# Kernel tuning notes

Hardware: AMD Instinct MI355X
Metric: run time of the kernel (lower is better)

Reference implementation:

```python
import jax, jax.numpy as jnp
import numpy as np

B, C, H, W = 4, 64, 64, 64
CI = C // 2  # inter_channels


def setup_inputs() -> dict:
    key = jax.random.key(0)
    k1, k2, k3, k4, k5 = jax.random.split(key, 5)
    x = jax.random.normal(k1, (B, C, H, W), dtype=jnp.float32)
    # 1x1 conv g: in C -> CI (weight [CI, C], bias [CI])
    Wg = jax.random.normal(k2, (CI, C), dtype=jnp.float32) * (1.0 / np.sqrt(C))
    bg = jax.random.normal(k3, (CI,), dtype=jnp.float32) * 0.01
    # 1x1 conv W_z: CI -> C
    Wz = jax.random.normal(k4, (C, CI), dtype=jnp.float32) * (1.0 / np.sqrt(CI))
    bz = jax.random.normal(k5, (C,), dtype=jnp.float32) * 0.01
    return {"x": x, "Wg": Wg, "bg": bg, "Wz": Wz, "bz": bz}


def reference(x, Wg, bg, Wz, bz):
    b, c, h, w = x.shape
    n = h * w
    xf = x.reshape(b, c, n)                       # [B,C,N]
    # g projection (1x1 conv) then flatten: [B,N,CI]
    g_x = jnp.einsum('bcn,oc->bno', xf, Wg) + bg  # [B,N,CI]
    # theta = phi = raw x flattened
    theta = xf.transpose(0, 2, 1)                 # [B,N,C]
    f = jnp.einsum('bnc,bcm->bnm', theta, xf)     # [B,N,N]
    f_div_C = jax.nn.softmax(f, axis=-1)
    y = jnp.einsum('bnm,bmo->bno', f_div_C, g_x)  # [B,N,CI]
    y = y.transpose(0, 2, 1).reshape(b, CI, h, w)  # [B,CI,H,W]
    # W_z projection (1x1 conv) + residual
    W_y = jnp.einsum('oi,bihw->bohw', Wz, y) + bz[None, :, None, None]
    return W_y + x
```

## Files before the change

### kernel.cpp

```cpp
#include <hip/hip_runtime.h>
#include <hip/hip_bf16.h>
#include <math.h>

#define B_  4
#define C_  64
#define N_  4096
#define CI_ 32
#define L2E 1.4426950408889634f

typedef __attribute__((ext_vector_type(8))) unsigned short u16x8;
typedef __attribute__((ext_vector_type(8))) __bf16        bf16x8;
typedef __attribute__((ext_vector_type(4))) float         f32x4;

union bfu { u16x8 u; bf16x8 b; };

__device__ __forceinline__ unsigned short f2bf(float f) {
    union { float f; unsigned int i; } v; v.f = f;
    unsigned int r = v.i + 0x7FFFu + ((v.i >> 16) & 1u);
    return (unsigned short)(r >> 16);
}

__global__ __launch_bounds__(256) void k_prep(
    const float* __restrict__ x, const float* __restrict__ Wg,
    const float* __restrict__ bg, unsigned short* __restrict__ xT,
    unsigned short* __restrict__ gx, float* __restrict__ diagS)
{
    __shared__ __align__(16) float tile[64][68];
    __shared__ float part[4][64][33];
    const int t  = threadIdx.x;
    const int b  = blockIdx.x >> 6;
    const int n0 = (blockIdx.x & 63) * 64;

    #pragma unroll
    for (int pass = 0; pass < 4; ++pass) {
        int c   = (t >> 4) + pass * 16;
        int nl4 = (t & 15) * 4;
        float4 v = *(const float4*)(x + (size_t)(b * C_ + c) * N_ + n0 + nl4);
        *(float4*)&tile[c][nl4] = v;
    }
    __syncthreads();

    {
        const int n  = t >> 2;
        const int cc = (t & 3) * 16;
        u16x8 a, b2;
        #pragma unroll
        for (int j = 0; j < 8; ++j) {
            a[j]  = f2bf(tile[cc + j][n]);
            b2[j] = f2bf(tile[cc + 8 + j][n]);
        }
        size_t off = (size_t)(b * N_ + n0 + n) * C_ + cc;
        *(u16x8*)(xT + off)     = a;
        *(u16x8*)(xT + off + 8) = b2;
    }
    {
        const int nl = t & 63, cq = t >> 6;
        float acc[CI_];
        #pragma unroll
        for (int o = 0; o < CI_; ++o) acc[o] = 0.f;
        float dd = 0.f;
        #pragma unroll 4
        for (int cl = 0; cl < 16; ++cl) {
            int c = cq * 16 + cl;
            float xv = tile[c][nl];
            dd += xv * xv;
            #pragma unroll
            for (int o = 0; o < CI_; ++o) acc[o] += Wg[o * C_ + c] * xv;
        }
        #pragma unroll
        for (int o = 0; o < CI_; ++o) part[cq][nl][o] = acc[o];
        part[cq][nl][32] = dd;
    }
    __syncthreads();
    {
        const int o = t >> 3, nr = (t & 7) * 8;
        u16x8 w;
        #pragma unroll
        for (int j = 0; j < 8; ++j) {
            int n = nr + j;
            float s = part[0][n][o] + part[1][n][o] + part[2][n][o] + part[3][n][o]
                    + bg[o];
            w[j] = f2bf(s);
        }
        *(u16x8*)(gx + (size_t)(b * CI_ + o) * N_ + n0 + nr) = w;
    }
    if (t < 64)
        diagS[(size_t)b * N_ + n0 + t] = L2E *
            (part[0][t][32] + part[1][t][32] + part[2][t][32] + part[3][t][32]);
}

__device__ __forceinline__ f32x4 mfma16(bf16x8 a, bf16x8 b, f32x4 c) {
    return __builtin_amdgcn_mfma_f32_16x16x32_bf16(a, b, c, 0, 0, 0);
}

__global__ __launch_bounds__(256, 3) void k_flash(
    const unsigned short* __restrict__ xT, const unsigned short* __restrict__ gx,
    const float* __restrict__ diagS,
    float* __restrict__ ypart, float* __restrict__ lpart)
{
    __shared__ __align__(16) char smem[34816];
    unsigned short* Pl = (unsigned short*)smem;
    float*          ym = (float*)smem;

    const int tid  = threadIdx.x;
    const int wave = tid >> 6, lane = tid & 63;
    const int quad = lane >> 4, li = lane & 15;
    const int bi  = blockIdx.x;
    const int kq  = bi & 3;
    const int qtb = (bi >> 2) & 63;
    const int b   = bi >> 8;
    const int q0  = qtb * 64;

    const unsigned short* xTb = xT + (size_t)b * N_ * C_;
    const unsigned short* gxb = gx + (size_t)(b * CI_) * N_;

    float nKq[4];
    #pragma unroll
    for (int qt = 0; qt < 4; ++qt)
        nKq[qt] = -diagS[(size_t)b * N_ + q0 + qt * 16 + li];

    bf16x8 Qf[4][2];
    #pragma unroll
    for (int qt = 0; qt < 4; ++qt)
        #pragma unroll
        for (int kc = 0; kc < 2; ++kc) {
            uint4 qr = *(const uint4*)(xTb + (size_t)(q0 + qt * 16 + li) * C_
                                       + kc * 32 + quad * 8);
            unsigned wv[4] = {qr.x, qr.y, qr.z, qr.w};
            bfu cv;
            #pragma unroll
            for (int j = 0; j < 4; ++j) {
                float lo = __uint_as_float(wv[j] << 16) * L2E;
                float hi = __uint_as_float(wv[j] & 0xFFFF0000u) * L2E;
                cv.u[2 * j]     = f2bf(lo);
                cv.u[2 * j + 1] = f2bf(hi);
            }
            Qf[qt][kc] = cv.b;
        }

    f32x4 Yf[4][2];
    #pragma unroll
    for (int qt = 0; qt < 4; ++qt)
        #pragma unroll
        for (int ot = 0; ot < 2; ++ot)
            Yf[qt][ot] = (f32x4){0.f, 0.f, 0.f, 0.f};
    float lacc[4] = {0.f, 0.f, 0.f, 0.f};

    const int keybase = kq * 1024 + wave * 256;

    for (int tl = 0; tl < 8; ++tl) {
        const int k0 = keybase + tl * 32;

        bf16x8 A[2][2];
        #pragma unroll
        for (int kt = 0; kt < 2; ++kt)
            #pragma unroll
            for (int kc = 0; kc < 2; ++kc)
                A[kt][kc] = *(const bf16x8*)(xTb + (size_t)(k0 + kt * 16 + li) * C_
                                             + kc * 32 + quad * 8);
        bf16x8 Bv[2];
        #pragma unroll
        for (int ot = 0; ot < 2; ++ot)
            Bv[ot] = *(const bf16x8*)(gxb + (size_t)(ot * 16 + li) * N_
                                      + k0 + quad * 8);

        #pragma unroll
        for (int kt = 0; kt < 2; ++kt) {
            f32x4 S[4];
            #pragma unroll
            for (int qt = 0; qt < 4; ++qt) {
                f32x4 z = (f32x4){nKq[qt], nKq[qt], nKq[qt], nKq[qt]};
                z = mfma16(A[kt][0], Qf[qt][0], z);
                S[qt] = mfma16(A[kt][1], Qf[qt][1], z);
            }
            #pragma unroll
            for (int qt = 0; qt < 4; ++qt) {
                float p[4];
                #pragma unroll
                for (int r = 0; r < 4; ++r) {
                    p[r] = __builtin_amdgcn_exp2f(S[qt][r]);
                    lacc[qt] += p[r];
                }
                uint2 wv;
                wv.x = __builtin_amdgcn_perm(__float_as_uint(p[1]),
                                             __float_as_uint(p[0]), 0x07060302);
                wv.y = __builtin_amdgcn_perm(__float_as_uint(p[3]),
                                             __float_as_uint(p[2]), 0x07060302);
                *(uint2*)(Pl + (wave * 64 + qt * 16 + li) * 40 + kt * 16 + quad * 4) = wv;
            }
        }

        #pragma unroll
        for (int qt = 0; qt < 4; ++qt) {
            bf16x8 Ap = *(const bf16x8*)(Pl + (wave * 64 + qt * 16 + li) * 40 + quad * 8);
            #pragma unroll
            for (int ot = 0; ot < 2; ++ot)
                Yf[qt][ot] = mfma16(Ap, Bv[ot], Yf[qt][ot]);
        }
    }

    #pragma unroll
    for (int qt = 0; qt < 4; ++qt) {
        lacc[qt] += __shfl_xor(lacc[qt], 16, 64);
        lacc[qt] += __shfl_xor(lacc[qt], 32, 64);
    }

    __syncthreads();
    #pragma unroll
    for (int qt = 0; qt < 4; ++qt) {
        #pragma unroll
        for (int ot = 0; ot < 2; ++ot)
            #pragma unroll
            for (int r = 0; r < 4; ++r)
                ym[(wave * 64 + qt * 16 + quad * 4 + r) * 34 + ot * 16 + li] = Yf[qt][ot][r];
        if (quad == 0)
            ym[(wave * 64 + qt * 16 + li) * 34 + 32] = lacc[qt];
    }
    __syncthreads();
    {
        const int q = tid >> 2, og = tid & 3;
        const size_t pbase = (size_t)(b * 64 + qtb) * 4 + kq;
        float* yp = ypart + pbase * 2048 + q * 32;
        #pragma unroll
        for (int j = 0; j < 8; ++j) {
            int o = og * 8 + j;
            yp[o] = ym[(0 * 64 + q) * 34 + o] + ym[(1 * 64 + q) * 34 + o]
                  + ym[(2 * 64 + q) * 34 + o] + ym[(3 * 64 + q) * 34 + o];
        }
        if (og == 0)
            lpart[pbase * 64 + q] = ym[(0 * 64 + q) * 34 + 32] + ym[(1 * 64 + q) * 34 + 32]
                                  + ym[(2 * 64 + q) * 34 + 32] + ym[(3 * 64 + q) * 34 + 32];
    }
}

__global__ __launch_bounds__(256) void k_merge(
    const float* __restrict__ ypart, const float* __restrict__ lpart,
    const float* __restrict__ x, const float* __restrict__ Wz,
    const float* __restrict__ bz, float* __restrict__ out)
{
    __shared__ float yfin[64][33];
    const int t   = threadIdx.x;
    const int b   = blockIdx.x >> 6;
    const int qtb = blockIdx.x & 63;
    const int q0  = qtb * 64;

    {
        const int q = t >> 2, og = t & 3;
        const size_t pb = (size_t)(b * 64 + qtb) * 4;
        float l = lpart[(pb + 0) * 64 + q] + lpart[(pb + 1) * 64 + q]
                + lpart[(pb + 2) * 64 + q] + lpart[(pb + 3) * 64 + q];
        float inv = 1.f / l;
        #pragma unroll
        for (int j = 0; j < 8; ++j) {
            int o = og * 8 + j;
            float acc = 0.f;
            #pragma unroll
            for (int kq = 0; kq < 4; ++kq)
                acc += ypart[(pb + kq) * 2048 + q * 32 + o];
            yfin[q][o] = acc * inv;
        }
    }
    __syncthreads();
    {
        const int q = t & 63, c0 = t >> 6;
        #pragma unroll
        for (int i = 0; i < 16; ++i) {
            int cout = c0 + i * 4;
            float acc = bz[cout];
            #pragma unroll
            for (int o = 0; o < CI_; ++o)
                acc += Wz[cout * CI_ + o] * yfin[q][o];
            size_t oidx = (size_t)(b * C_ + cout) * N_ + q0 + q;
            out[oidx] = acc + x[oidx];
        }
    }
}

extern "C" void kernel_launch(void* const* d_in, const int* in_sizes, int n_in,
                              void* d_out, int out_size, void* d_ws, size_t ws_size,
                              hipStream_t stream) {
    (void)in_sizes; (void)n_in; (void)out_size; (void)ws_size;
    const float* x  = (const float*)d_in[0];
    const float* Wg = (const float*)d_in[1];
    const float* bg = (const float*)d_in[2];
    const float* Wz = (const float*)d_in[3];
    const float* bz = (const float*)d_in[4];
    float* out = (float*)d_out;

    unsigned short* xT = (unsigned short*)d_ws;
    unsigned short* gx = (unsigned short*)((char*)d_ws + 2097152);
    float* diagS = (float*)((char*)d_ws + 3145728);
    float* ypart = (float*)((char*)d_ws + 3211264);
    float* lpart = (float*)((char*)d_ws + 11599872);

    hipLaunchKernelGGL(k_prep,  dim3(B_ * (N_ / 64)), dim3(256), 0, stream,
                       x, Wg, bg, xT, gx, diagS);
    hipLaunchKernelGGL(k_flash, dim3(B_ * 64 * 4),    dim3(256), 0, stream,
                       xT, gx, diagS, ypart, lpart);
    hipLaunchKernelGGL(k_merge, dim3(B_ * 64),        dim3(256), 0, stream,
                       ypart, lpart, x, Wz, bz, out);
}
```

Before: 124.0 us.

## Shrink prep/merge tiles to 16 columns and double-buffer flash key loads

k_prep and k_merge now handle 16 spatial positions per block instead of 64, giving 4x more blocks with lighter per-thread work. Both use vectorized float4 loads for weights, partial results and the residual. k_flash prefetches the next key tile's xT and gx fragments into a second register buffer while the current tile is computed, to hide global load latency. The aim is better GPU occupancy in the small kernels and overlapped loads in the main one, at the cost of more registers in k_flash and less reuse of Wg/Wz per block.

```diff
diff --git a/kernel.cpp b/kernel.cpp
--- a/kernel.cpp
+++ b/kernel.cpp
@@ -9,6 +9,7 @@
 #define L2E 1.4426950408889634f
 
 typedef __attribute__((ext_vector_type(8))) unsigned short u16x8;
+typedef __attribute__((ext_vector_type(4))) unsigned short u16x4;
 typedef __attribute__((ext_vector_type(8))) __bf16        bf16x8;
 typedef __attribute__((ext_vector_type(4))) float         f32x4;
 
@@ -25,68 +26,53 @@
     const float* __restrict__ bg, unsigned short* __restrict__ xT,
     unsigned short* __restrict__ gx, float* __restrict__ diagS)
 {
-    __shared__ __align__(16) float tile[64][68];
-    __shared__ float part[4][64][33];
+    __shared__ __align__(16) float tile[64][20];
+    __shared__ unsigned short gout[CI_][16];
     const int t  = threadIdx.x;
-    const int b  = blockIdx.x >> 6;
-    const int n0 = (blockIdx.x & 63) * 64;
-
-    #pragma unroll
-    for (int pass = 0; pass < 4; ++pass) {
-        int c   = (t >> 4) + pass * 16;
-        int nl4 = (t & 15) * 4;
-        float4 v = *(const float4*)(x + (size_t)(b * C_ + c) * N_ + n0 + nl4);
-        *(float4*)&tile[c][nl4] = v;
-    }
-    __syncthreads();
-
-    {
-        const int n  = t >> 2;
-        const int cc = (t & 3) * 16;
-        u16x8 a, b2;
-        #pragma unroll
-        for (int j = 0; j < 8; ++j) {
-            a[j]  = f2bf(tile[cc + j][n]);
-            b2[j] = f2bf(tile[cc + 8 + j][n]);
-        }
-        size_t off = (size_t)(b * N_ + n0 + n) * C_ + cc;
-        *(u16x8*)(xT + off)     = a;
-        *(u16x8*)(xT + off + 8) = b2;
-    }
-    {
-        const int nl = t & 63, cq = t >> 6;
-        float acc[CI_];
-        #pragma unroll
-        for (int o = 0; o < CI_; ++o) acc[o] = 0.f;
-        float dd = 0.f;
-        #pragma unroll 4
-        for (int cl = 0; cl < 16; ++cl) {
-            int c = cq * 16 + cl;
-            float xv = tile[c][nl];
-            dd += xv * xv;
-            #pragma unroll
-            for (int o = 0; o < CI_; ++o) acc[o] += Wg[o * C_ + c] * xv;
-        }
-        #pragma unroll
-        for (int o = 0; o < CI_; ++o) part[cq][nl][o] = acc[o];
-        part[cq][nl][32] = dd;
-    }
-    __syncthreads();
-    {
-        const int o = t >> 3, nr = (t & 7) * 8;
-        u16x8 w;
-        #pragma unroll
-        for (int j = 0; j < 8; ++j) {
-            int n = nr + j;
-            float s = part[0][n][o] + part[1][n][o] + part[2][n][o] + part[3][n][o]
-                    + bg[o];
-            w[j] = f2bf(s);
-        }
-        *(u16x8*)(gx + (size_t)(b * CI_ + o) * N_ + n0 + nr) = w;
-    }
-    if (t < 64)
-        diagS[(size_t)b * N_ + n0 + t] = L2E *
-            (part[0][t][32] + part[1][t][32] + part[2][t][32] + part[3][t][32]);
+    const int b  = blockIdx.x >> 8;
+    const int n0 = (blockIdx.x & 255) * 16;
+
+    {
+        const int c  = t >> 2;
+        const int nq = (t & 3) * 4;
+        float4 v = *(const float4*)(x + (size_t)(b * C_ + c) * N_ + n0 + nq);
+        *(float4*)&tile[c][nq] = v;
+    }
+    __syncthreads();
+
+    {
+        const int cg = t & 15, n = t >> 4;
+        u16x4 w;
+        #pragma unroll
+        for (int j = 0; j < 4; ++j) w[j] = f2bf(tile[cg * 4 + j][n]);
+        *(u16x4*)(xT + (size_t)(b * N_ + n0 + n) * C_ + cg * 4) = w;
+    }
+    {
+        const int n = t >> 4, oh = t & 15;
+        const int o0 = oh * 2, o1 = o0 + 1;
+        float a0 = 0.f, a1 = 0.f, dd = 0.f;
+        #pragma unroll
+        for (int c4 = 0; c4 < 16; ++c4) {
+            float4 w0 = *(const float4*)(Wg + o0 * C_ + c4 * 4);
+            float4 w1 = *(const float4*)(Wg + o1 * C_ + c4 * 4);
+            float x0 = tile[c4 * 4 + 0][n], x1 = tile[c4 * 4 + 1][n];
+            float x2 = tile[c4 * 4 + 2][n], x3 = tile[c4 * 4 + 3][n];
+            a0 += w0.x * x0 + w0.y * x1 + w0.z * x2 + w0.w * x3;
+            a1 += w1.x * x0 + w1.y * x1 + w1.z * x2 + w1.w * x3;
+            dd += x0 * x0 + x1 * x1 + x2 * x2 + x3 * x3;
+        }
+        gout[o0][n] = f2bf(a0 + bg[o0]);
+        gout[o1][n] = f2bf(a1 + bg[o1]);
+        if (oh == 0) diagS[(size_t)b * N_ + n0 + n] = L2E * dd;
+    }
+    __syncthreads();
+    if (t < 128) {
+        const int o = t >> 2, n4 = (t & 3) * 4;
+        u16x4 w;
+        #pragma unroll
+        for (int j = 0; j < 4; ++j) w[j] = gout[o][n4 + j];
+        *(u16x4*)(gx + (size_t)(b * CI_ + o) * N_ + n0 + n4) = w;
+    }
 }
 
 __device__ __forceinline__ f32x4 mfma16(bf16x8 a, bf16x8 b, f32x4 c) {
@@ -148,21 +134,26 @@
 
     const int keybase = kq * 1024 + wave * 256;
 
+    auto load_tile = [&](int k0, bf16x8 Ad[2][2], bf16x8 Bd[2]) {
+        #pragma unroll
+        for (int kt = 0; kt < 2; ++kt)
+            #pragma unroll
+            for (int kc = 0; kc < 2; ++kc)
+                Ad[kt][kc] = *(const bf16x8*)(xTb + (size_t)(k0 + kt * 16 + li) * C_
+                                              + kc * 32 + quad * 8);
+        #pragma unroll
+        for (int ot = 0; ot < 2; ++ot)
+            Bd[ot] = *(const bf16x8*)(gxb + (size_t)(ot * 16 + li) * N_
+                                      + k0 + quad * 8);
+    };
+
+    bf16x8 Ab[2][2][2], Bb[2][2];
+    load_tile(keybase, Ab[0], Bb[0]);
+
+    #pragma unroll
     for (int tl = 0; tl < 8; ++tl) {
-        const int k0 = keybase + tl * 32;
-
-        bf16x8 A[2][2];
-        #pragma unroll
-        for (int kt = 0; kt < 2; ++kt)
-            #pragma unroll
-            for (int kc = 0; kc < 2; ++kc)
-                A[kt][kc] = *(const bf16x8*)(xTb + (size_t)(k0 + kt * 16 + li) * C_
-                                             + kc * 32 + quad * 8);
-        bf16x8 Bv[2];
-        #pragma unroll
-        for (int ot = 0; ot < 2; ++ot)
-            Bv[ot] = *(const bf16x8*)(gxb + (size_t)(ot * 16 + li) * N_
-                                      + k0 + quad * 8);
+        const int cur = tl & 1, nxt = cur ^ 1;
+        if (tl < 7) load_tile(keybase + (tl + 1) * 32, Ab[nxt], Bb[nxt]);
 
         #pragma unroll
         for (int kt = 0; kt < 2; ++kt) {
@@ -170,8 +161,8 @@
             #pragma unroll
             for (int qt = 0; qt < 4; ++qt) {
                 f32x4 z = (f32x4){nKq[qt], nKq[qt], nKq[qt], nKq[qt]};
-                z = mfma16(A[kt][0], Qf[qt][0], z);
-                S[qt] = mfma16(A[kt][1], Qf[qt][1], z);
+                z = mfma16(Ab[cur][kt][0], Qf[qt][0], z);
+                S[qt] = mfma16(Ab[cur][kt][1], Qf[qt][1], z);
             }
             #pragma unroll
             for (int qt = 0; qt < 4; ++qt) {
@@ -195,7 +186,7 @@
             bf16x8 Ap = *(const bf16x8*)(Pl + (wave * 64 + qt * 16 + li) * 40 + quad * 8);
             #pragma unroll
             for (int ot = 0; ot < 2; ++ot)
-                Yf[qt][ot] = mfma16(Ap, Bv[ot], Yf[qt][ot]);
+                Yf[qt][ot] = mfma16(Ap, Bb[cur][ot], Yf[qt][ot]);
         }
     }
 
@@ -238,41 +229,51 @@
     const float* __restrict__ x, const float* __restrict__ Wz,
     const float* __restrict__ bz, float* __restrict__ out)
 {
-    __shared__ float yfin[64][33];
+    __shared__ __align__(16) float yfin[16][36];
     const int t   = threadIdx.x;
-    const int b   = blockIdx.x >> 6;
-    const int qtb = blockIdx.x & 63;
-    const int q0  = qtb * 64;
-
-    {
-        const int q = t >> 2, og = t & 3;
-        const size_t pb = (size_t)(b * 64 + qtb) * 4;
-        float l = lpart[(pb + 0) * 64 + q] + lpart[(pb + 1) * 64 + q]
-                + lpart[(pb + 2) * 64 + q] + lpart[(pb + 3) * 64 + q];
+    const int b   = blockIdx.x >> 8;
+    const int qt  = blockIdx.x & 255;
+    const int q0  = qt * 16;
+    const int qtb64 = qt >> 2, sub = qt & 3;
+    const size_t pb = (size_t)(b * 64 + qtb64) * 4;
+
+    if (t < 128) {
+        const int q = t >> 3, o4 = (t & 7) * 4;
+        const int q64 = sub * 16 + q;
+        float l = lpart[(pb + 0) * 64 + q64] + lpart[(pb + 1) * 64 + q64]
+                + lpart[(pb + 2) * 64 + q64] + lpart[(pb + 3) * 64 + q64];
         float inv = 1.f / l;
-        #pragma unroll
-        for (int j = 0; j < 8; ++j) {
-            int o = og * 8 + j;
-            float acc = 0.f;
-            #pragma unroll
-            for (int kq = 0; kq < 4; ++kq)
-                acc += ypart[(pb + kq) * 2048 + q * 32 + o];
-            yfin[q][o] = acc * inv;
-        }
-    }
-    __syncthreads();
-    {
-        const int q = t & 63, c0 = t >> 6;
-        #pragma unroll
-        for (int i = 0; i < 16; ++i) {
-            int cout = c0 + i * 4;
-            float acc = bz[cout];
-            #pragma unroll
-            for (int o = 0; o < CI_; ++o)
-                acc += Wz[cout * CI_ + o] * yfin[q][o];
-            size_t oidx = (size_t)(b * C_ + cout) * N_ + q0 + q;
-            out[oidx] = acc + x[oidx];
-        }
+        float4 acc = (float4){0.f, 0.f, 0.f, 0.f};
+        #pragma unroll
+        for (int kq = 0; kq < 4; ++kq) {
+            float4 v = *(const float4*)(ypart + (pb + kq) * 2048 + q64 * 32 + o4);
+            acc.x += v.x; acc.y += v.y; acc.z += v.z; acc.w += v.w;
+        }
+        yfin[q][o4 + 0] = acc.x * inv;
+        yfin[q][o4 + 1] = acc.y * inv;
+        yfin[q][o4 + 2] = acc.z * inv;
+        yfin[q][o4 + 3] = acc.w * inv;
+    }
+    __syncthreads();
+    {
+        const int c = t >> 2, qg = t & 3;
+        float acc[4];
+        float bzv = bz[c];
+        #pragma unroll
+        for (int j = 0; j < 4; ++j) acc[j] = bzv;
+        #pragma unroll
+        for (int o4 = 0; o4 < 8; ++o4) {
+            float4 wz = *(const float4*)(Wz + c * CI_ + o4 * 4);
+            #pragma unroll
+            for (int j = 0; j < 4; ++j) {
+                const float* yr = &yfin[qg * 4 + j][o4 * 4];
+                acc[j] += wz.x * yr[0] + wz.y * yr[1] + wz.z * yr[2] + wz.w * yr[3];
+            }
+        }
+        size_t oidx = (size_t)(b * C_ + c) * N_ + q0 + qg * 4;
+        float4 xr = *(const float4*)(x + oidx);
+        float4 ov = (float4){acc[0] + xr.x, acc[1] + xr.y, acc[2] + xr.z, acc[3] + xr.w};
+        *(float4*)(out + oidx) = ov;
     }
 }
 
@@ -293,10 +294,10 @@
     float* ypart = (float*)((char*)d_ws + 3211264);
     float* lpart = (float*)((char*)d_ws + 11599872);
 
-    hipLaunchKernelGGL(k_prep,  dim3(B_ * (N_ / 64)), dim3(256), 0, stream,
+    hipLaunchKernelGGL(k_prep,  dim3(B_ * 256),    dim3(256), 0, stream,
                        x, Wg, bg, xT, gx, diagS);
-    hipLaunchKernelGGL(k_flash, dim3(B_ * 64 * 4),    dim3(256), 0, stream,
+    hipLaunchKernelGGL(k_flash, dim3(B_ * 64 * 4), dim3(256), 0, stream,
                        xT, gx, diagS, ypart, lpart);
-    hipLaunchKernelGGL(k_merge, dim3(B_ * 64),        dim3(256), 0, stream,
+    hipLaunchKernelGGL(k_merge, dim3(B_ * 256),    dim3(256), 0, stream,
                        ypart, lpart, x, Wz, bz, out);
 }
```

After: 118.1 us. -4.8%, faster.
